# Kernel optimization log

Measured on AMD Instinct MI355X. Metric: run time of the kernel, lower is better.

The kernel has to match this reference:

```python
import jax, jax.numpy as jnp
import numpy as np

DIM = 180
HEADS = 6
HEAD_DIM = DIM // HEADS  # 30
WS = 16                  # window size
PWS = WS // 2            # permuted window size (8)
N = WS * WS              # 256 tokens per window
M = PWS * PWS            # 64 pooled kv tokens per window
B = 4                    # batch (images)
NW = 256                 # windows per image
BW = B * NW              # total windows (b_)
SCALE = HEAD_DIM ** -0.5


def _aligned_rel_index():
    # replicates the buffer construction in __init__ (torch.meshgrid default = 'ij')
    coords = np.stack(np.meshgrid(np.arange(PWS), np.arange(PWS), indexing='ij'))
    cf = coords.reshape(2, -1)
    rel = (cf[:, :, None] - cf[:, None, :]).transpose(1, 2, 0).copy()
    rel[:, :, 0] += PWS - 1
    rel[:, :, 1] += PWS - 1
    rel[:, :, 0] *= 2 * PWS - 1
    idx = rel.sum(-1)  # (M, M)
    idx = idx.reshape(PWS, PWS, 1, 1, M)
    idx = np.tile(idx, (1, 1, 2, 2, 1)).transpose(0, 2, 1, 3, 4).reshape(4 * M, M)
    return idx  # (N, M)


def setup_inputs() -> dict:
    key = jax.random.key(0)
    ks = jax.random.split(key, 10)
    num_bias = (2 * PWS - 1) * (2 * PWS - 1)  # 225
    inp = {
        'x': jax.random.normal(ks[0], (BW, N, DIM), jnp.float32),
        'k_v': jax.random.normal(ks[1], (B, 256), jnp.float32),
        'mask': jnp.zeros((NW, N, M), jnp.float32),
        'W_kernel': jax.random.normal(ks[2], (DIM * 2, 256), jnp.float32) * 0.02,
        'W_q': jax.random.normal(ks[3], (DIM, DIM), jnp.float32) * 0.02,
        'b_q': jnp.zeros((DIM,), jnp.float32),
        'W_kv': jax.random.normal(ks[4], (DIM // 2, DIM), jnp.float32) * 0.02,
        'b_kv': jnp.zeros((DIM // 2,), jnp.float32),
        'bias_table': jax.random.normal(ks[5], (num_bias, HEADS), jnp.float32) * 0.02,
        'W_proj': jax.random.normal(ks[6], (DIM, DIM), jnp.float32) * 0.02,
        'b_proj': jnp.zeros((DIM,), jnp.float32),
        'rel_index': jnp.asarray(_aligned_rel_index(), jnp.int32),
        'b': B,
        'windows_size': WS,
    }
    return inp


def reference(x, k_v, mask, W_kernel, W_q, b_q, W_kv, b_kv, bias_table,
              W_proj, b_proj, rel_index, b, windows_size):
    b_, n, c = x.shape
    # FiLM-style modulation: per-image scale/shift broadcast over all windows/tokens
    kv_mod = (k_v @ W_kernel.T).reshape(-1, 1, 1, 1, c * 2)   # (b,1,1,1,2c)
    k_v1, k_v2 = jnp.split(kv_mod, 2, axis=4)
    xr = x.reshape(b, -1, windows_size, windows_size, c)
    x = (xr * k_v1 + k_v2).reshape(b_, n, c)

    # pooled kv: 2x2 spatial pool packed into channels, split into k and v
    kv = (x @ W_kv.T + b_kv)
    kv = kv.reshape(b_, PWS, 2, PWS, 2, 2, c // 4)
    kv = kv.transpose(0, 1, 3, 5, 2, 4, 6).reshape(b_, n // 4, 2, HEADS, c // HEADS)
    kv = kv.transpose(2, 0, 3, 1, 4)                          # (2, b_, h, n//4, d)
    k, v = kv[0], kv[1]

    q = (x @ W_q.T + b_q).reshape(b_, n, HEADS, HEAD_DIM).transpose(0, 2, 1, 3)
    q = q * SCALE                                             # (b_, h, n, d)

    attn = jnp.einsum('bhnd,bhmd->bhnm', q, k)                # (b_, h, n, n//4)

    # gathered relative position bias
    rpb = bias_table[rel_index.reshape(-1)].reshape(n, n // 4, HEADS)
    attn = attn + rpb.transpose(2, 0, 1)[None]

    nw = mask.shape[0]
    attn = attn.reshape(b_ // nw, nw, HEADS, n, n // 4) + mask[None, :, None]
    attn = attn.reshape(-1, HEADS, n, n // 4)
    attn = jax.nn.softmax(attn, axis=-1)

    out = jnp.einsum('bhnm,bhmd->bhnd', attn, v)
    out = out.transpose(0, 2, 1, 3).reshape(b_, n, c)
    return out @ W_proj.T + b_proj
```

## Files before the change

kernel.cpp:

```cpp
#include <hip/hip_runtime.h>
#include <stdint.h>


#define NHEADS 6
#define SCALE_Q 0.18257418583505536f

#define KVM_OFF   0
#define WCAT_OFF  1440
#define WPROJ_OFF 29088
#define BCAT_OFF  47520
#define RPB_OFF   47808

typedef _Float16 f16x8 __attribute__((ext_vector_type(8)));
typedef float    f32x4 __attribute__((ext_vector_type(4)));

__device__ __forceinline__ uint32_t pkf16(float lo, float hi) {
    return __builtin_bit_cast(uint32_t, __builtin_amdgcn_cvt_pkrtz(lo, hi));
}
__device__ __forceinline__ unsigned short f16b(float v) {
    return __builtin_bit_cast(unsigned short, (_Float16)v);
}
__device__ __forceinline__ f32x4 mfma16(f16x8 a, f16x8 b, f32x4 c) {
    return __builtin_amdgcn_mfma_f32_16x16x32_f16(a, b, c, 0, 0, 0);
}

__global__ __launch_bounds__(256) void prep_kernel(
    const float* __restrict__ k_v, const float* __restrict__ W_kernel,
    const float* __restrict__ W_q, const float* __restrict__ b_q,
    const float* __restrict__ W_kv, const float* __restrict__ b_kv,
    const float* __restrict__ W_proj, const float* __restrict__ bias_table,
    const int* __restrict__ rel_index, float* __restrict__ ws)
{
    const int bid = blockIdx.x, tid = threadIdx.x;
    uint32_t* wsd = (uint32_t*)ws;
    if (bid < 6) {
        const int j = bid * 256 + tid;
        if (j < 1440) {
            const int img = j / 360;
            const int o = j - img * 360;
            const float* kr = k_v + img * 256;
            const float* wr = W_kernel + o * 256;
            float s0 = 0.f, s1 = 0.f, s2 = 0.f, s3 = 0.f;
            for (int t = 0; t < 256; t += 4) {
                s0 = fmaf(kr[t + 0], wr[t + 0], s0);
                s1 = fmaf(kr[t + 1], wr[t + 1], s1);
                s2 = fmaf(kr[t + 2], wr[t + 2], s2);
                s3 = fmaf(kr[t + 3], wr[t + 3], s3);
            }
            ws[KVM_OFF + j] = (s0 + s1) + (s2 + s3);
        }
    } else if (bid < 114) {
        const int i = (bid - 6) * 256 + tid;
        if (i < 27648) {
            const int j = i / 96, k0 = (i - j * 96) * 2;
            float v0 = 0.f, v1 = 0.f;
            if (j < 180) {
                if (k0 < 180)     v0 = W_q[j * 180 + k0] * SCALE_Q;
                if (k0 + 1 < 180) v1 = W_q[j * 180 + k0 + 1] * SCALE_Q;
            } else if (j < 270) {
                const int jj = j - 180;
                if (k0 < 180)     v0 = W_kv[jj * 180 + k0];
                if (k0 + 1 < 180) v1 = W_kv[jj * 180 + k0 + 1];
            }
            wsd[WCAT_OFF + i] = pkf16(v0, v1);
        }
    } else if (bid < 186) {
        const int i = (bid - 114) * 256 + tid;
        if (i < 18432) {
            const int j = i / 96, k0 = (i - j * 96) * 2;
            float v0 = (j < 180 && k0 < 180)     ? W_proj[j * 180 + k0]     : 0.f;
            float v1 = (j < 180 && k0 + 1 < 180) ? W_proj[j * 180 + k0 + 1] : 0.f;
            wsd[WPROJ_OFF + i] = pkf16(v0, v1);
        }
    } else if (bid == 186) {
        if (tid < 288) {
            float b = 0.f;
            if (tid < 180)      b = b_q[tid] * SCALE_Q;
            else if (tid < 270) b = b_kv[tid - 180];
            ws[BCAT_OFF + tid] = b;
        }
    } else {
        const int i = (bid - 187) * 256 + tid;
        if (i < 98304) {
            const int t = i & 255, m = (i >> 8) & 63, h = i >> 14;
            ws[RPB_OFF + i] = bias_table[rel_index[t * 64 + m] * NHEADS + h];
        }
    }
}

__global__ __launch_bounds__(512, 2) void fused_all(
    const float* __restrict__ x, const float* __restrict__ mask,
    const float* __restrict__ ws_f, const float* __restrict__ b_proj,
    float* __restrict__ out)
{
    __shared__ __attribute__((aligned(16))) char U[81920];
    char* Kls = U;
    char* Vt  = U + 24576;
    char* Scr = U + 49152;
    char* As  = U;

    const int tid = threadIdx.x;
    const int win = blockIdx.x;
    const int img = win >> 8;
    const int w   = win & 255;
    const int lane = tid & 63, wv = tid >> 6;
    const int lr = lane & 15, lk = lane >> 4;
    const int wrow = wv * 32;

    const uint32_t* wsd = (const uint32_t*)ws_f;
    const _Float16* wcat  = (const _Float16*)(wsd + WCAT_OFF);
    const _Float16* wproj = (const _Float16*)(wsd + WPROJ_OFF);
    const float*    kvs   = ws_f + KVM_OFF + img * 360;
    const float*    bcat  = ws_f + BCAT_OFF;

    if (tid < 384) {
        const int h = tid >> 6, mm = tid & 63;
        *(uint32_t*)(Kls + h * 4096 + mm * 64 + ((3u ^ ((mm >> 1) & 3)) << 4) + 12) = 0u;
    }

    const float* xr0 = x + ((size_t)win * 256 + wrow + lr) * 180;
    const float* xr1 = xr0 + 16 * 180;

    auto load_af = [&](const float* xrow, int c0) -> f16x8 {
        union { uint32_t u[4]; f16x8 v; } cv;
        if (c0 + 8 <= 180) {
            float4 a  = *(const float4*)(xrow + c0);
            float4 b  = *(const float4*)(xrow + c0 + 4);
            float4 s0 = *(const float4*)(kvs + c0);
            float4 s1 = *(const float4*)(kvs + c0 + 4);
            float4 h0 = *(const float4*)(kvs + 180 + c0);
            float4 h1 = *(const float4*)(kvs + 180 + c0 + 4);
            cv.u[0] = pkf16(fmaf(a.x, s0.x, h0.x), fmaf(a.y, s0.y, h0.y));
            cv.u[1] = pkf16(fmaf(a.z, s0.z, h0.z), fmaf(a.w, s0.w, h0.w));
            cv.u[2] = pkf16(fmaf(b.x, s1.x, h1.x), fmaf(b.y, s1.y, h1.y));
            cv.u[3] = pkf16(fmaf(b.z, s1.z, h1.z), fmaf(b.w, s1.w, h1.w));
        } else if (c0 < 180) {
            float4 a  = *(const float4*)(xrow + 176);
            float4 s0 = *(const float4*)(kvs + 176);
            float4 h0 = *(const float4*)(kvs + 356);
            cv.u[0] = pkf16(fmaf(a.x, s0.x, h0.x), fmaf(a.y, s0.y, h0.y));
            cv.u[1] = pkf16(fmaf(a.z, s0.z, h0.z), fmaf(a.w, s0.w, h0.w));
            cv.u[2] = 0u; cv.u[3] = 0u;
        } else {
            cv.u[0] = cv.u[1] = cv.u[2] = cv.u[3] = 0u;
        }
        return cv.v;
    };

    f16x8 xa[2][6];
#pragma unroll
    for (int kk = 0; kk < 6; ++kk) {
        const int c0 = kk * 32 + lk * 8;
        xa[0][kk] = load_af(xr0, c0);
        xa[1][kk] = load_af(xr1, c0);
    }

    auto run6 = [&](int cb, f32x4 (&acc)[2][6]) {
#pragma unroll
        for (int kk = 0; kk < 6; ++kk) {
#pragma unroll
            for (int nf = 0; nf < 6; ++nf) {
                f16x8 bf = *(const f16x8*)(wcat + (size_t)(cb + nf * 16 + lr) * 192 + kk * 32 + lk * 8);
                acc[0][nf] = mfma16(xa[0][kk], bf, acc[0][nf]);
                acc[1][nf] = mfma16(xa[1][kk], bf, acc[1][nf]);
            }
        }
    };

    {
        f32x4 akv[2][6];
#pragma unroll
        for (int a = 0; a < 2; ++a)
#pragma unroll
            for (int b = 0; b < 6; ++b) akv[a][b] = (f32x4){0.f, 0.f, 0.f, 0.f};
        run6(176, akv);
#pragma unroll
        for (int nf = 0; nf < 6; ++nf) {
            const int col = 176 + nf * 16 + lr;
            const int j = col - 180;
            if (j >= 0 && j < 90) {
                const float bb = bcat[col];
                const int d45 = (j < 45) ? j : j - 45;
#pragma unroll
                for (int mf = 0; mf < 2; ++mf)
#pragma unroll
                    for (int rr = 0; rr < 4; ++rr) {
                        const int t = wrow + mf * 16 + lk * 4 + rr;
                        const int mm = ((t >> 5) << 3) + ((t >> 1) & 7);
                        const int base = ((t >> 4) & 1) * 90 + (t & 1) * 45;
                        const int flat = base + d45;
                        const int h = (flat * 2185) >> 16;
                        const int d = flat - h * 30;
                        const unsigned short hv = f16b(akv[mf][nf][rr] + bb);
                        if (j < 45)
                            *(unsigned short*)(Kls + h * 4096 + mm * 64 +
                                ((((unsigned)d >> 3) ^ ((mm >> 1) & 3)) << 4) + (d & 7) * 2) = hv;
                        else
                            *(unsigned short*)(Vt + h * 4096 + d * 128 +
                                ((((unsigned)mm >> 3) ^ (d & 7)) << 4) + (mm & 7) * 2) = hv;
                    }
            }
        }
    }

    uint32_t qp[2][12][2];
#pragma unroll
    for (int half = 0; half < 2; ++half) {
        f32x4 aq[2][6];
#pragma unroll
        for (int a = 0; a < 2; ++a)
#pragma unroll
            for (int b = 0; b < 6; ++b) aq[a][b] = (f32x4){0.f, 0.f, 0.f, 0.f};
        run6(half * 96, aq);
#pragma unroll
        for (int nf = 0; nf < 6; ++nf) {
            const float bb = bcat[half * 96 + nf * 16 + lr];
#pragma unroll
            for (int mf = 0; mf < 2; ++mf) {
                qp[mf][half * 6 + nf][0] = pkf16(aq[mf][nf][0] + bb, aq[mf][nf][1] + bb);
                qp[mf][half * 6 + nf][1] = pkf16(aq[mf][nf][2] + bb, aq[mf][nf][3] + bb);
            }
        }
    }

    __syncthreads();

    char* scr = Scr + wv * 4096;
    char* Pw  = scr + 2048;
    const float* rpbt = ws_f + RPB_OFF;

    if (lane < 32)
        *(uint32_t*)(scr + lane * 64 + ((3u ^ ((lane >> 1) & 3)) << 4) + 12) = 0u;

    uint32_t opk[2][NHEADS][4];

#pragma unroll
    for (int qt = 0; qt < 2; ++qt) {
        const int t0 = wrow + qt * 16 + lk * 4;

#pragma unroll
        for (int h = 0; h < NHEADS; ++h) {
#pragma unroll
            for (int nf = 0; nf < 12; ++nf) {
                if (nf * 16 + 15 >= 30 * h && nf * 16 < 30 * h + 30) {
                    const int d = nf * 16 + lr - 30 * h;
                    if (d >= 0 && d < 30) {
#pragma unroll
                        for (int rp = 0; rp < 2; ++rp) {
                            const int rL = qt * 16 + lk * 4 + rp * 2;
                            char* p0 = scr + rL * 64 +
                                ((((unsigned)d >> 3) ^ ((rL >> 1) & 3)) << 4) + (d & 7) * 2;
                            const uint32_t q2 = qp[qt][nf][rp];
                            *(unsigned short*)p0        = (unsigned short)(q2 & 0xffffu);
                            *(unsigned short*)(p0 + 64) = (unsigned short)(q2 >> 16);
                        }
                    }
                }
            }

            const int rq = qt * 16 + lr;
            f16x8 qf = *(const f16x8*)(scr + rq * 64 +
                (((unsigned)lk ^ ((rq >> 1) & 3)) << 4));

            f32x4 sa[4];
#pragma unroll
            for (int mt = 0; mt < 4; ++mt) {
                const int m = mt * 16 + lr;
                const float4 rv = *(const float4*)(rpbt + (((size_t)(h * 64 + m)) << 8) + t0);
                const float* mk = mask + ((((size_t)w << 8) + t0) << 6) + m;
                sa[mt][0] = rv.x + mk[0];
                sa[mt][1] = rv.y + mk[64];
                sa[mt][2] = rv.z + mk[128];
                sa[mt][3] = rv.w + mk[192];
            }

#pragma unroll
            for (int mt = 0; mt < 4; ++mt) {
                const int mm = mt * 16 + lr;
                f16x8 kf = *(const f16x8*)(Kls + h * 4096 + mm * 64 +
                    (((unsigned)lk ^ ((mm >> 1) & 3)) << 4));
                sa[mt] = mfma16(qf, kf, sa[mt]);
            }

            float mx[4], sm[4], inv[4];
#pragma unroll
            for (int rr = 0; rr < 4; ++rr)
                mx[rr] = fmaxf(fmaxf(sa[0][rr], sa[1][rr]), fmaxf(sa[2][rr], sa[3][rr]));
#pragma unroll
            for (int xm = 1; xm < 16; xm <<= 1)
#pragma unroll
                for (int rr = 0; rr < 4; ++rr)
                    mx[rr] = fmaxf(mx[rr], __shfl_xor(mx[rr], xm));
#pragma unroll
            for (int mt = 0; mt < 4; ++mt)
#pragma unroll
                for (int rr = 0; rr < 4; ++rr)
                    sa[mt][rr] = __expf(sa[mt][rr] - mx[rr]);
#pragma unroll
            for (int rr = 0; rr < 4; ++rr)
                sm[rr] = (sa[0][rr] + sa[1][rr]) + (sa[2][rr] + sa[3][rr]);
#pragma unroll
            for (int xm = 1; xm < 16; xm <<= 1)
#pragma unroll
                for (int rr = 0; rr < 4; ++rr)
                    sm[rr] += __shfl_xor(sm[rr], xm);
#pragma unroll
            for (int rr = 0; rr < 4; ++rr) inv[rr] = 1.0f / sm[rr];

#pragma unroll
            for (int mt = 0; mt < 4; ++mt) {
                const int m = mt * 16 + lr;
#pragma unroll
                for (int rr = 0; rr < 4; ++rr) {
                    const int r16 = lk * 4 + rr;
                    *(unsigned short*)(Pw + r16 * 128 +
                        ((((unsigned)m >> 3) ^ (r16 & 7)) << 4) + (m & 7) * 2) = f16b(sa[mt][rr]);
                }
            }

            f32x4 oa[2];
            oa[0] = (f32x4){0.f, 0.f, 0.f, 0.f};
            oa[1] = (f32x4){0.f, 0.f, 0.f, 0.f};
#pragma unroll
            for (int ks = 0; ks < 2; ++ks) {
                f16x8 pa = *(const f16x8*)(Pw + lr * 128 +
                    ((((unsigned)(ks * 4 + lk)) ^ (lr & 7)) << 4));
#pragma unroll
                for (int df = 0; df < 2; ++df) {
                    const int d = df * 16 + lr;
                    f16x8 vb = *(const f16x8*)(Vt + h * 4096 + d * 128 +
                        ((((unsigned)(ks * 4 + lk)) ^ (d & 7)) << 4));
                    oa[df] = mfma16(pa, vb, oa[df]);
                }
            }

#pragma unroll
            for (int df = 0; df < 2; ++df) {
                opk[qt][h][df * 2 + 0] = pkf16(oa[df][0] * inv[0], oa[df][1] * inv[1]);
                opk[qt][h][df * 2 + 1] = pkf16(oa[df][2] * inv[2], oa[df][3] * inv[3]);
            }
        }
    }

    auto stage32 = [&]() {
        const int rbase = (wv & 3) * 32;
#pragma unroll
        for (int qt = 0; qt < 2; ++qt)
#pragma unroll
            for (int h = 0; h < NHEADS; ++h)
#pragma unroll
                for (int df = 0; df < 2; ++df) {
                    const int d = df * 16 + lr;
                    if (d < 30) {
                        const int col = h * 30 + d;
#pragma unroll
                        for (int p = 0; p < 2; ++p) {
                            const uint32_t v = opk[qt][h][df * 2 + p];
                            const int r0 = rbase + qt * 16 + lk * 4 + p * 2;
                            char* a0 = As + r0 * 384 +
                                ((((unsigned)col >> 3) ^ (r0 & 7)) << 4) + (col & 7) * 2;
                            char* a1 = As + (r0 + 1) * 384 +
                                ((((unsigned)col >> 3) ^ ((r0 + 1) & 7)) << 4) + (col & 7) * 2;
                            *(unsigned short*)a0 = (unsigned short)(v & 0xffffu);
                            *(unsigned short*)a1 = (unsigned short)(v >> 16);
                        }
                    }
                }
        if (lane < 32) {
            const int r = rbase + lane;
            *(uint2*)(As + r * 384 + ((22u ^ (unsigned)(r & 7)) << 4) + 8) = (uint2){0u, 0u};
            *(uint4*)(As + r * 384 + ((23u ^ (unsigned)(r & 7)) << 4)) = (uint4){0u, 0u, 0u, 0u};
        }
    };

    auto proj_half = [&](int half) {
        f32x4 acc[12];
#pragma unroll
        for (int nf = 0; nf < 12; ++nf) acc[nf] = (f32x4){0.f, 0.f, 0.f, 0.f};
#pragma unroll
        for (int kk = 0; kk < 6; ++kk) {
            const int r = wv * 16 + lr;
            f16x8 af = *(const f16x8*)(As + r * 384 +
                ((((unsigned)(kk * 4 + lk)) ^ (r & 7)) << 4));
#pragma unroll
            for (int nf = 0; nf < 12; ++nf) {
                f16x8 bf = *(const f16x8*)(wproj + (size_t)(nf * 16 + lr) * 192 + kk * 32 + lk * 8);
                acc[nf] = mfma16(af, bf, acc[nf]);
            }
        }
#pragma unroll
        for (int nf = 0; nf < 12; ++nf) {
            const int j = nf * 16 + lr;
            if (j < 180) {
                const float bb = b_proj[j];
                const size_t row = (size_t)win * 256 + half * 128 + wv * 16 + lk * 4;
#pragma unroll
                for (int rr = 0; rr < 4; ++rr)
                    out[(row + rr) * 180 + j] = acc[nf][rr] + bb;
            }
        }
    };

    __syncthreads();
    if (wv < 4) stage32();
    __syncthreads();
    proj_half(0);
    __syncthreads();
    if (wv >= 4) stage32();
    __syncthreads();
    proj_half(1);
}

extern "C" void kernel_launch(void* const* d_in, const int* in_sizes, int n_in,
                              void* d_out, int out_size, void* d_ws, size_t ws_size,
                              hipStream_t stream)
{
    (void)in_sizes; (void)n_in; (void)out_size; (void)ws_size;
    const float* x          = (const float*)d_in[0];
    const float* k_v        = (const float*)d_in[1];
    const float* mask       = (const float*)d_in[2];
    const float* W_kernel   = (const float*)d_in[3];
    const float* W_q        = (const float*)d_in[4];
    const float* b_q        = (const float*)d_in[5];
    const float* W_kv       = (const float*)d_in[6];
    const float* b_kv       = (const float*)d_in[7];
    const float* bias_table = (const float*)d_in[8];
    const float* W_proj     = (const float*)d_in[9];
    const float* b_proj     = (const float*)d_in[10];
    const int*   rel_index  = (const int*)d_in[11];

    float* ws = (float*)d_ws;

    prep_kernel<<<571, 256, 0, stream>>>(k_v, W_kernel, W_q, b_q, W_kv, b_kv,
                                         W_proj, bias_table, rel_index, ws);
    fused_all<<<1024, 512, 0, stream>>>(x, mask, ws, b_proj, (float*)d_out);
}
```

Before: 455.9 us.

## Use 1024-thread blocks with 16 rows per wave in fused attention

Doubles the block size to 16 waves so each wave handles 16 token rows instead of 32, halving per-wave register arrays (inputs, accumulators, q and output packs). The projection stage splits output columns across wave pairs, and shared scratch grows to hold 16 per-wave scratch buffers. The aim is more waves in flight to hide memory and MFMA latency. In exchange, each wave's weight fragment loads are amortized over fewer rows, and the larger shared-memory footprint may limit how many blocks fit per CU.

Result: slower. 537.3 us (+17.9%).

```diff
diff --git a/kernel.cpp b/kernel.cpp
--- a/kernel.cpp
+++ b/kernel.cpp
@@ -88,12 +88,12 @@
     }
 }
 
-__global__ __launch_bounds__(512, 2) void fused_all(
+__global__ __launch_bounds__(1024, 4) void fused_all(
     const float* __restrict__ x, const float* __restrict__ mask,
     const float* __restrict__ ws_f, const float* __restrict__ b_proj,
     float* __restrict__ out)
 {
-    __shared__ __attribute__((aligned(16))) char U[81920];
+    __shared__ __attribute__((aligned(16))) char U[98304];
     char* Kls = U;
     char* Vt  = U + 24576;
     char* Scr = U + 49152;
@@ -105,7 +105,7 @@
     const int w   = win & 255;
     const int lane = tid & 63, wv = tid >> 6;
     const int lr = lane & 15, lk = lane >> 4;
-    const int wrow = wv * 32;
+    const int wrow = wv * 16;
 
     const uint32_t* wsd = (const uint32_t*)ws_f;
     const _Float16* wcat  = (const _Float16*)(wsd + WCAT_OFF);
@@ -119,7 +119,6 @@
     }
 
     const float* xr0 = x + ((size_t)win * 256 + wrow + lr) * 180;
-    const float* xr1 = xr0 + 16 * 180;
 
     auto load_af = [&](const float* xrow, int c0) -> f16x8 {
         union { uint32_t u[4]; f16x8 v; } cv;
@@ -147,32 +146,26 @@
         return cv.v;
     };
 
-    f16x8 xa[2][6];
-#pragma unroll
-    for (int kk = 0; kk < 6; ++kk) {
-        const int c0 = kk * 32 + lk * 8;
-        xa[0][kk] = load_af(xr0, c0);
-        xa[1][kk] = load_af(xr1, c0);
-    }
-
-    auto run6 = [&](int cb, f32x4 (&acc)[2][6]) {
+    f16x8 xa[6];
+#pragma unroll
+    for (int kk = 0; kk < 6; ++kk)
+        xa[kk] = load_af(xr0, kk * 32 + lk * 8);
+
+    auto run6 = [&](int cb, f32x4 (&acc)[6]) {
 #pragma unroll
         for (int kk = 0; kk < 6; ++kk) {
 #pragma unroll
             for (int nf = 0; nf < 6; ++nf) {
                 f16x8 bf = *(const f16x8*)(wcat + (size_t)(cb + nf * 16 + lr) * 192 + kk * 32 + lk * 8);
-                acc[0][nf] = mfma16(xa[0][kk], bf, acc[0][nf]);
-                acc[1][nf] = mfma16(xa[1][kk], bf, acc[1][nf]);
+                acc[nf] = mfma16(xa[kk], bf, acc[nf]);
             }
         }
     };
 
     {
-        f32x4 akv[2][6];
-#pragma unroll
-        for (int a = 0; a < 2; ++a)
-#pragma unroll
-            for (int b = 0; b < 6; ++b) akv[a][b] = (f32x4){0.f, 0.f, 0.f, 0.f};
+        f32x4 akv[6];
+#pragma unroll
+        for (int b = 0; b < 6; ++b) akv[b] = (f32x4){0.f, 0.f, 0.f, 0.f};
         run6(176, akv);
 #pragma unroll
         for (int nf = 0; nf < 6; ++nf) {
@@ -182,191 +175,177 @@
                 const float bb = bcat[col];
                 const int d45 = (j < 45) ? j : j - 45;
 #pragma unroll
-                for (int mf = 0; mf < 2; ++mf)
-#pragma unroll
-                    for (int rr = 0; rr < 4; ++rr) {
-                        const int t = wrow + mf * 16 + lk * 4 + rr;
-                        const int mm = ((t >> 5) << 3) + ((t >> 1) & 7);
-                        const int base = ((t >> 4) & 1) * 90 + (t & 1) * 45;
-                        const int flat = base + d45;
-                        const int h = (flat * 2185) >> 16;
-                        const int d = flat - h * 30;
-                        const unsigned short hv = f16b(akv[mf][nf][rr] + bb);
-                        if (j < 45)
-                            *(unsigned short*)(Kls + h * 4096 + mm * 64 +
-                                ((((unsigned)d >> 3) ^ ((mm >> 1) & 3)) << 4) + (d & 7) * 2) = hv;
-                        else
-                            *(unsigned short*)(Vt + h * 4096 + d * 128 +
-                                ((((unsigned)mm >> 3) ^ (d & 7)) << 4) + (mm & 7) * 2) = hv;
-                    }
+                for (int rr = 0; rr < 4; ++rr) {
+                    const int t = wrow + lk * 4 + rr;
+                    const int mm = ((t >> 5) << 3) + ((t >> 1) & 7);
+                    const int base = ((t >> 4) & 1) * 90 + (t & 1) * 45;
+                    const int flat = base + d45;
+                    const int h = (flat * 2185) >> 16;
+                    const int d = flat - h * 30;
+                    const unsigned short hv = f16b(akv[nf][rr] + bb);
+                    if (j < 45)
+                        *(unsigned short*)(Kls + h * 4096 + mm * 64 +
+                            ((((unsigned)d >> 3) ^ ((mm >> 1) & 3)) << 4) + (d & 7) * 2) = hv;
+                    else
+                        *(unsigned short*)(Vt + h * 4096 + d * 128 +
+                            ((((unsigned)mm >> 3) ^ (d & 7)) << 4) + (mm & 7) * 2) = hv;
+                }
             }
         }
     }
 
-    uint32_t qp[2][12][2];
+    uint32_t qp[12][2];
 #pragma unroll
     for (int half = 0; half < 2; ++half) {
-        f32x4 aq[2][6];
-#pragma unroll
-        for (int a = 0; a < 2; ++a)
-#pragma unroll
-            for (int b = 0; b < 6; ++b) aq[a][b] = (f32x4){0.f, 0.f, 0.f, 0.f};
+        f32x4 aq[6];
+#pragma unroll
+        for (int b = 0; b < 6; ++b) aq[b] = (f32x4){0.f, 0.f, 0.f, 0.f};
         run6(half * 96, aq);
 #pragma unroll
         for (int nf = 0; nf < 6; ++nf) {
             const float bb = bcat[half * 96 + nf * 16 + lr];
-#pragma unroll
-            for (int mf = 0; mf < 2; ++mf) {
-                qp[mf][half * 6 + nf][0] = pkf16(aq[mf][nf][0] + bb, aq[mf][nf][1] + bb);
-                qp[mf][half * 6 + nf][1] = pkf16(aq[mf][nf][2] + bb, aq[mf][nf][3] + bb);
-            }
+            qp[half * 6 + nf][0] = pkf16(aq[nf][0] + bb, aq[nf][1] + bb);
+            qp[half * 6 + nf][1] = pkf16(aq[nf][2] + bb, aq[nf][3] + bb);
         }
     }
 
     __syncthreads();
 
-    char* scr = Scr + wv * 4096;
-    char* Pw  = scr + 2048;
+    char* scr = Scr + wv * 3072;
+    char* Pw  = scr + 1024;
     const float* rpbt = ws_f + RPB_OFF;
 
-    if (lane < 32)
+    if (lane < 16)
         *(uint32_t*)(scr + lane * 64 + ((3u ^ ((lane >> 1) & 3)) << 4) + 12) = 0u;
 
-    uint32_t opk[2][NHEADS][4];
-
-#pragma unroll
-    for (int qt = 0; qt < 2; ++qt) {
-        const int t0 = wrow + qt * 16 + lk * 4;
-
-#pragma unroll
-        for (int h = 0; h < NHEADS; ++h) {
-#pragma unroll
-            for (int nf = 0; nf < 12; ++nf) {
-                if (nf * 16 + 15 >= 30 * h && nf * 16 < 30 * h + 30) {
-                    const int d = nf * 16 + lr - 30 * h;
-                    if (d >= 0 && d < 30) {
-#pragma unroll
-                        for (int rp = 0; rp < 2; ++rp) {
-                            const int rL = qt * 16 + lk * 4 + rp * 2;
-                            char* p0 = scr + rL * 64 +
-                                ((((unsigned)d >> 3) ^ ((rL >> 1) & 3)) << 4) + (d & 7) * 2;
-                            const uint32_t q2 = qp[qt][nf][rp];
-                            *(unsigned short*)p0        = (unsigned short)(q2 & 0xffffu);
-                            *(unsigned short*)(p0 + 64) = (unsigned short)(q2 >> 16);
-                        }
+    uint32_t opk[NHEADS][4];
+    const int t0 = wrow + lk * 4;
+
+#pragma unroll
+    for (int h = 0; h < NHEADS; ++h) {
+#pragma unroll
+        for (int nf = 0; nf < 12; ++nf) {
+            if (nf * 16 + 15 >= 30 * h && nf * 16 < 30 * h + 30) {
+                const int d = nf * 16 + lr - 30 * h;
+                if (d >= 0 && d < 30) {
+#pragma unroll
+                    for (int rp = 0; rp < 2; ++rp) {
+                        const int rL = lk * 4 + rp * 2;
+                        char* p0 = scr + rL * 64 +
+                            ((((unsigned)d >> 3) ^ ((rL >> 1) & 3)) << 4) + (d & 7) * 2;
+                        const uint32_t q2 = qp[nf][rp];
+                        *(unsigned short*)p0        = (unsigned short)(q2 & 0xffffu);
+                        *(unsigned short*)(p0 + 64) = (unsigned short)(q2 >> 16);
                     }
                 }
             }
-
-            const int rq = qt * 16 + lr;
-            f16x8 qf = *(const f16x8*)(scr + rq * 64 +
-                (((unsigned)lk ^ ((rq >> 1) & 3)) << 4));
-
-            f32x4 sa[4];
-#pragma unroll
-            for (int mt = 0; mt < 4; ++mt) {
-                const int m = mt * 16 + lr;
-                const float4 rv = *(const float4*)(rpbt + (((size_t)(h * 64 + m)) << 8) + t0);
-                const float* mk = mask + ((((size_t)w << 8) + t0) << 6) + m;
-                sa[mt][0] = rv.x + mk[0];
-                sa[mt][1] = rv.y + mk[64];
-                sa[mt][2] = rv.z + mk[128];
-                sa[mt][3] = rv.w + mk[192];
-            }
-
-#pragma unroll
-            for (int mt = 0; mt < 4; ++mt) {
-                const int mm = mt * 16 + lr;
-                f16x8 kf = *(const f16x8*)(Kls + h * 4096 + mm * 64 +
-                    (((unsigned)lk ^ ((mm >> 1) & 3)) << 4));
-                sa[mt] = mfma16(qf, kf, sa[mt]);
-            }
-
-            float mx[4], sm[4], inv[4];
+        }
+
+        f16x8 qf = *(const f16x8*)(scr + lr * 64 +
+            (((unsigned)lk ^ ((lr >> 1) & 3)) << 4));
+
+        f32x4 sa[4];
+#pragma unroll
+        for (int mt = 0; mt < 4; ++mt) {
+            const int m = mt * 16 + lr;
+            const float4 rv = *(const float4*)(rpbt + (((size_t)(h * 64 + m)) << 8) + t0);
+            const float* mk = mask + ((((size_t)w << 8) + t0) << 6) + m;
+            sa[mt][0] = rv.x + mk[0];
+            sa[mt][1] = rv.y + mk[64];
+            sa[mt][2] = rv.z + mk[128];
+            sa[mt][3] = rv.w + mk[192];
+        }
+
+#pragma unroll
+        for (int mt = 0; mt < 4; ++mt) {
+            const int mm = mt * 16 + lr;
+            f16x8 kf = *(const f16x8*)(Kls + h * 4096 + mm * 64 +
+                (((unsigned)lk ^ ((mm >> 1) & 3)) << 4));
+            sa[mt] = mfma16(qf, kf, sa[mt]);
+        }
+
+        float mx[4], sm[4], inv[4];
+#pragma unroll
+        for (int rr = 0; rr < 4; ++rr)
+            mx[rr] = fmaxf(fmaxf(sa[0][rr], sa[1][rr]), fmaxf(sa[2][rr], sa[3][rr]));
+#pragma unroll
+        for (int xm = 1; xm < 16; xm <<= 1)
 #pragma unroll
             for (int rr = 0; rr < 4; ++rr)
-                mx[rr] = fmaxf(fmaxf(sa[0][rr], sa[1][rr]), fmaxf(sa[2][rr], sa[3][rr]));
-#pragma unroll
-            for (int xm = 1; xm < 16; xm <<= 1)
-#pragma unroll
-                for (int rr = 0; rr < 4; ++rr)
-                    mx[rr] = fmaxf(mx[rr], __shfl_xor(mx[rr], xm));
-#pragma unroll
-            for (int mt = 0; mt < 4; ++mt)
-#pragma unroll
-                for (int rr = 0; rr < 4; ++rr)
-                    sa[mt][rr] = __expf(sa[mt][rr] - mx[rr]);
+                mx[rr] = fmaxf(mx[rr], __shfl_xor(mx[rr], xm));
+#pragma unroll
+        for (int mt = 0; mt < 4; ++mt)
 #pragma unroll
             for (int rr = 0; rr < 4; ++rr)
-                sm[rr] = (sa[0][rr] + sa[1][rr]) + (sa[2][rr] + sa[3][rr]);
-#pragma unroll
-            for (int xm = 1; xm < 16; xm <<= 1)
-#pragma unroll
-                for (int rr = 0; rr < 4; ++rr)
-                    sm[rr] += __shfl_xor(sm[rr], xm);
-#pragma unroll
-            for (int rr = 0; rr < 4; ++rr) inv[rr] = 1.0f / sm[rr];
-
-#pragma unroll
-            for (int mt = 0; mt < 4; ++mt) {
-                const int m = mt * 16 + lr;
-#pragma unroll
-                for (int rr = 0; rr < 4; ++rr) {
-                    const int r16 = lk * 4 + rr;
-                    *(unsigned short*)(Pw + r16 * 128 +
-                        ((((unsigned)m >> 3) ^ (r16 & 7)) << 4) + (m & 7) * 2) = f16b(sa[mt][rr]);
-                }
-            }
-
-            f32x4 oa[2];
-            oa[0] = (f32x4){0.f, 0.f, 0.f, 0.f};
-            oa[1] = (f32x4){0.f, 0.f, 0.f, 0.f};
-#pragma unroll
-            for (int ks = 0; ks < 2; ++ks) {
-                f16x8 pa = *(const f16x8*)(Pw + lr * 128 +
-                    ((((unsigned)(ks * 4 + lk)) ^ (lr & 7)) << 4));
-#pragma unroll
-                for (int df = 0; df < 2; ++df) {
-                    const int d = df * 16 + lr;
-                    f16x8 vb = *(const f16x8*)(Vt + h * 4096 + d * 128 +
-                        ((((unsigned)(ks * 4 + lk)) ^ (d & 7)) << 4));
-                    oa[df] = mfma16(pa, vb, oa[df]);
-                }
-            }
-
+                sa[mt][rr] = __expf(sa[mt][rr] - mx[rr]);
+#pragma unroll
+        for (int rr = 0; rr < 4; ++rr)
+            sm[rr] = (sa[0][rr] + sa[1][rr]) + (sa[2][rr] + sa[3][rr]);
+#pragma unroll
+        for (int xm = 1; xm < 16; xm <<= 1)
+#pragma unroll
+            for (int rr = 0; rr < 4; ++rr)
+                sm[rr] += __shfl_xor(sm[rr], xm);
+#pragma unroll
+        for (int rr = 0; rr < 4; ++rr) inv[rr] = 1.0f / sm[rr];
+
+#pragma unroll
+        for (int mt = 0; mt < 4; ++mt) {
+            const int m = mt * 16 + lr;
+#pragma unroll
+            for (int rr = 0; rr < 4; ++rr) {
+                const int r16 = lk * 4 + rr;
+                *(unsigned short*)(Pw + r16 * 128 +
+                    ((((unsigned)m >> 3) ^ (r16 & 7)) << 4) + (m & 7) * 2) = f16b(sa[mt][rr]);
+            }
+        }
+
+        f32x4 oa[2];
+        oa[0] = (f32x4){0.f, 0.f, 0.f, 0.f};
+        oa[1] = (f32x4){0.f, 0.f, 0.f, 0.f};
+#pragma unroll
+        for (int ks = 0; ks < 2; ++ks) {
+            f16x8 pa = *(const f16x8*)(Pw + lr * 128 +
+                ((((unsigned)(ks * 4 + lk)) ^ (lr & 7)) << 4));
 #pragma unroll
             for (int df = 0; df < 2; ++df) {
-                opk[qt][h][df * 2 + 0] = pkf16(oa[df][0] * inv[0], oa[df][1] * inv[1]);
-                opk[qt][h][df * 2 + 1] = pkf16(oa[df][2] * inv[2], oa[df][3] * inv[3]);
-            }
+                const int d = df * 16 + lr;
+                f16x8 vb = *(const f16x8*)(Vt + h * 4096 + d * 128 +
+                    ((((unsigned)(ks * 4 + lk)) ^ (d & 7)) << 4));
+                oa[df] = mfma16(pa, vb, oa[df]);
+            }
+        }
+
+#pragma unroll
+        for (int df = 0; df < 2; ++df) {
+            opk[h][df * 2 + 0] = pkf16(oa[df][0] * inv[0], oa[df][1] * inv[1]);
+            opk[h][df * 2 + 1] = pkf16(oa[df][2] * inv[2], oa[df][3] * inv[3]);
         }
     }
 
-    auto stage32 = [&]() {
-        const int rbase = (wv & 3) * 32;
-#pragma unroll
-        for (int qt = 0; qt < 2; ++qt)
-#pragma unroll
-            for (int h = 0; h < NHEADS; ++h)
-#pragma unroll
-                for (int df = 0; df < 2; ++df) {
-                    const int d = df * 16 + lr;
-                    if (d < 30) {
-                        const int col = h * 30 + d;
-#pragma unroll
-                        for (int p = 0; p < 2; ++p) {
-                            const uint32_t v = opk[qt][h][df * 2 + p];
-                            const int r0 = rbase + qt * 16 + lk * 4 + p * 2;
-                            char* a0 = As + r0 * 384 +
-                                ((((unsigned)col >> 3) ^ (r0 & 7)) << 4) + (col & 7) * 2;
-                            char* a1 = As + (r0 + 1) * 384 +
-                                ((((unsigned)col >> 3) ^ ((r0 + 1) & 7)) << 4) + (col & 7) * 2;
-                            *(unsigned short*)a0 = (unsigned short)(v & 0xffffu);
-                            *(unsigned short*)a1 = (unsigned short)(v >> 16);
-                        }
+    auto stage16 = [&]() {
+        const int rbase = (wv & 7) * 16;
+#pragma unroll
+        for (int h = 0; h < NHEADS; ++h)
+#pragma unroll
+            for (int df = 0; df < 2; ++df) {
+                const int d = df * 16 + lr;
+                if (d < 30) {
+                    const int col = h * 30 + d;
+#pragma unroll
+                    for (int p = 0; p < 2; ++p) {
+                        const uint32_t v = opk[h][df * 2 + p];
+                        const int r0 = rbase + lk * 4 + p * 2;
+                        char* a0 = As + r0 * 384 +
+                            ((((unsigned)col >> 3) ^ (r0 & 7)) << 4) + (col & 7) * 2;
+                        char* a1 = As + (r0 + 1) * 384 +
+                            ((((unsigned)col >> 3) ^ ((r0 + 1) & 7)) << 4) + (col & 7) * 2;
+                        *(unsigned short*)a0 = (unsigned short)(v & 0xffffu);
+                        *(unsigned short*)a1 = (unsigned short)(v >> 16);
                     }
                 }
-        if (lane < 32) {
+            }
+        if (lane < 16) {
             const int r = rbase + lane;
             *(uint2*)(As + r * 384 + ((22u ^ (unsigned)(r & 7)) << 4) + 8) = (uint2){0u, 0u};
             *(uint4*)(As + r * 384 + ((23u ^ (unsigned)(r & 7)) << 4)) = (uint4){0u, 0u, 0u, 0u};
@@ -374,26 +353,28 @@
     };
 
     auto proj_half = [&](int half) {
-        f32x4 acc[12];
-#pragma unroll
-        for (int nf = 0; nf < 12; ++nf) acc[nf] = (f32x4){0.f, 0.f, 0.f, 0.f};
+        const int rblk = wv >> 1, chalf = wv & 1;
+        f32x4 acc[6];
+#pragma unroll
+        for (int nf = 0; nf < 6; ++nf) acc[nf] = (f32x4){0.f, 0.f, 0.f, 0.f};
 #pragma unroll
         for (int kk = 0; kk < 6; ++kk) {
-            const int r = wv * 16 + lr;
+            const int r = rblk * 16 + lr;
             f16x8 af = *(const f16x8*)(As + r * 384 +
                 ((((unsigned)(kk * 4 + lk)) ^ (r & 7)) << 4));
 #pragma unroll
-            for (int nf = 0; nf < 12; ++nf) {
-                f16x8 bf = *(const f16x8*)(wproj + (size_t)(nf * 16 + lr) * 192 + kk * 32 + lk * 8);
+            for (int nf = 0; nf < 6; ++nf) {
+                f16x8 bf = *(const f16x8*)(wproj +
+                    (size_t)(chalf * 96 + nf * 16 + lr) * 192 + kk * 32 + lk * 8);
                 acc[nf] = mfma16(af, bf, acc[nf]);
             }
         }
 #pragma unroll
-        for (int nf = 0; nf < 12; ++nf) {
-            const int j = nf * 16 + lr;
+        for (int nf = 0; nf < 6; ++nf) {
+            const int j = chalf * 96 + nf * 16 + lr;
             if (j < 180) {
                 const float bb = b_proj[j];
-                const size_t row = (size_t)win * 256 + half * 128 + wv * 16 + lk * 4;
+                const size_t row = (size_t)win * 256 + half * 128 + rblk * 16 + lk * 4;
 #pragma unroll
                 for (int rr = 0; rr < 4; ++rr)
                     out[(row + rr) * 180 + j] = acc[nf][rr] + bb;
@@ -402,11 +383,11 @@
     };
 
     __syncthreads();
-    if (wv < 4) stage32();
+    if (wv < 8) stage16();
     __syncthreads();
     proj_half(0);
     __syncthreads();
-    if (wv >= 4) stage32();
+    if (wv >= 8) stage16();
     __syncthreads();
     proj_half(1);
 }
@@ -433,5 +414,5 @@
 
     prep_kernel<<<571, 256, 0, stream>>>(k_v, W_kernel, W_q, b_q, W_kv, b_kv,
                                          W_proj, bias_table, rel_index, ws);
-    fused_all<<<1024, 512, 0, stream>>>(x, mask, ws, b_proj, (float*)d_out);
-}
+    fused_all<<<1024, 1024, 0, stream>>>(x, mask, ws, b_proj, (float*)d_out);
+}
```
